# Performance work log

Measured on AMD Instinct MI355X. Metric: run time of the kernel, lower is better.

The kernel has to match this reference:

```python
import jax, jax.numpy as jnp
import numpy as np

N_HIDDEN = 32
RANK = 6
SV_DECAY_GAMMA = 0.3
LEAK_ALPHA = 0.1
INPUT_DIM = 64
OUTPUT_DIM = 32


def setup_inputs() -> dict:
    key = jax.random.key(0)
    ks = jax.random.split(key, 8)
    B, T = 256, 2048
    inputs = jax.random.normal(ks[0], (B, T, INPUT_DIM), dtype=jnp.float32)
    # parameters (match torch init scales)
    m = jax.random.normal(ks[1], (N_HIDDEN, 1), dtype=jnp.float32) * 0.1
    n = jax.random.normal(ks[2], (N_HIDDEN, 1), dtype=jnp.float32) * 0.1
    M = jax.random.normal(ks[3], (N_HIDDEN, RANK), dtype=jnp.float32) * 0.1
    Nmat = jax.random.normal(ks[4], (N_HIDDEN, RANK), dtype=jnp.float32) * 0.1
    # singular-value-decay scaling of M, N (as in _initialize_with_sv_decay)
    target_sv = jnp.exp(-SV_DECAY_GAMMA * jnp.arange(RANK, dtype=jnp.float32))
    target_sv = target_sv / target_sv.sum() * RANK
    sqrt_sv = jnp.sqrt(target_sv)
    M = M * sqrt_sv[None, :]
    Nmat = Nmat * sqrt_sv[None, :]
    bias = jnp.zeros((N_HIDDEN,), dtype=jnp.float32)
    # W_in: Linear(input_dim, N, bias=False) -> weight [N, input_dim]
    lim_in = 1.0 / np.sqrt(INPUT_DIM)
    W_in = jax.random.uniform(ks[5], (N_HIDDEN, INPUT_DIM), minval=-lim_in, maxval=lim_in, dtype=jnp.float32)
    lim_out = 1.0 / np.sqrt(N_HIDDEN)
    W_out = jax.random.uniform(ks[6], (OUTPUT_DIM, N_HIDDEN), minval=-lim_out, maxval=lim_out, dtype=jnp.float32)
    b_out = jax.random.uniform(ks[7], (OUTPUT_DIM,), minval=-lim_out, maxval=lim_out, dtype=jnp.float32)
    return {"inputs": inputs, "W_in": W_in, "m": m, "n": n, "M": M,
            "Nmat": Nmat, "bias": bias, "W_out": W_out, "b_out": b_out}


def reference(inputs, W_in, m, n, M, Nmat, bias, W_out, b_out):
    # h_{t+1} = (1-a) h_t + a * tanh(W_rec h_t + W_in u_t + b); y_t = W_out h_t + b_out
    B, T, _ = inputs.shape
    alpha = LEAK_ALPHA
    # W_rec = m n^T + M N^T (time-invariant; torch recomputes per step, same math)
    W_rec = m @ n.T + M @ Nmat.T                         # [N, N]
    x_proj = jnp.einsum('bti,ni->btn', inputs, W_in)     # [B, T, N]
    h0 = jnp.zeros((B, N_HIDDEN), dtype=inputs.dtype)

    def step(h, x_t):
        pre = h @ W_rec.T + x_t + bias
        h_new = (1.0 - alpha) * h + alpha * jnp.tanh(pre)
        return h_new, h_new

    h_final, hs = jax.lax.scan(step, h0, jnp.swapaxes(x_proj, 0, 1))  # hs: [T, B, N]
    outputs = jnp.einsum('tbn,on->bto', hs, W_out) + b_out            # [B, T, O]
    return outputs, h_final
```

## Files before the change

### kernel.cpp

```cpp
#include <hip/hip_runtime.h>

#define RNN_B 256
#define RNN_T 2048
#define RNN_IN 64
#define RNN_N 32
#define RNN_O 32
#define RNN_R 6
#define RNN_ALPHA 0.1f
#define KSCALE 2.8853900817779268f

__global__ __launch_bounds__(256) void k_xproj(
    const float* __restrict__ u, const float* __restrict__ W_in,
    const float* __restrict__ bias, float* __restrict__ xp)
{
    const int tid = blockIdx.x * 256 + threadIdx.x;
    const float4* __restrict__ u4 =
        reinterpret_cast<const float4*>(u) + (size_t)tid * (RNN_IN / 4);
    float acc[RNN_N];
    #pragma unroll
    for (int n = 0; n < RNN_N; ++n) acc[n] = bias[n];
    #pragma unroll
    for (int q = 0; q < RNN_IN / 4; ++q) {
        const float4 v = u4[q];
        #pragma unroll
        for (int n = 0; n < RNN_N; ++n) {
            const float* wr = W_in + n * RNN_IN + 4 * q;
            acc[n] = fmaf(wr[0], v.x, acc[n]);
            acc[n] = fmaf(wr[1], v.y, acc[n]);
            acc[n] = fmaf(wr[2], v.z, acc[n]);
            acc[n] = fmaf(wr[3], v.w, acc[n]);
        }
    }
    float4* __restrict__ o4 =
        reinterpret_cast<float4*>(xp) + (size_t)tid * (RNN_N / 4);
    #pragma unroll
    for (int q = 0; q < RNN_N / 4; ++q)
        o4[q] = make_float4(KSCALE * acc[4*q+0], KSCALE * acc[4*q+1],
                            KSCALE * acc[4*q+2], KSCALE * acc[4*q+3]);
}

template <int CTRL>
__device__ __forceinline__ float dpp_add(float v) {
    int t = __builtin_amdgcn_update_dpp(0, __float_as_int(v), CTRL, 0xf, 0xf, true);
    return v + __int_as_float(t);
}
__device__ __forceinline__ float sum16(float v) {
    v = dpp_add<0xB1>(v);
    v = dpp_add<0x4E>(v);
    v = dpp_add<0x141>(v);
    v = dpp_add<0x140>(v);
    return v;
}

__device__ __forceinline__ float xsum32(float v) {
#if __has_builtin(__builtin_amdgcn_permlane32_swap)
    typedef int v2i __attribute__((ext_vector_type(2)));
    v2i r = __builtin_amdgcn_permlane32_swap(__float_as_int(v),
                                             __float_as_int(v), false, false);
    return __int_as_float(r.x) + __int_as_float(r.y);
#else
    return v + __shfl_xor(v, 32, 64);
#endif
}
__device__ __forceinline__ float xsum16(float v) {
#if __has_builtin(__builtin_amdgcn_permlane16_swap)
    typedef int v2i __attribute__((ext_vector_type(2)));
    v2i r = __builtin_amdgcn_permlane16_swap(__float_as_int(v),
                                             __float_as_int(v), false, false);
    return __int_as_float(r.x) + __int_as_float(r.y);
#else
    return v + __shfl_xor(v, 16, 64);
#endif
}

__device__ __forceinline__ float fast_exp2(float x) {
#if __has_builtin(__builtin_amdgcn_exp2f)
    return __builtin_amdgcn_exp2f(x);
#else
    return __expf(x * 0.6931471805599453f);
#endif
}
__device__ __forceinline__ float fast_rcp(float x) {
#if __has_builtin(__builtin_amdgcn_rcpf)
    return __builtin_amdgcn_rcpf(x);
#else
    return __frcp_rn(x);
#endif
}

__global__ __launch_bounds__(64, 1) void k_recur(
    const float* __restrict__ m, const float* __restrict__ nvec,
    const float* __restrict__ Mmat, const float* __restrict__ Nmat,
    const float* __restrict__ xp,
    float* __restrict__ hout,
    float* __restrict__ hfin)
{
    const int b    = blockIdx.x;
    const int lane = threadIdx.x;
    const int k    = lane & 15;
    const int q    = (lane >> 4) & 1;
    const int p    = lane >> 5;
    const int e    = 2 * k + p;

    float cn[4], cm[4];
    #pragma unroll
    for (int j = 0; j < 4; ++j) {
        const int r = 4 * q + j;
        float cnv = 0.f, cmv = 0.f;
        if (r == 0)      { cnv = nvec[e];              cmv = m[e]; }
        else if (r <= RNN_R) { cnv = Nmat[e*RNN_R + (r-1)]; cmv = Mmat[e*RNN_R + (r-1)]; }
        cn[j] = cnv;
        cm[j] = KSCALE * cmv;
    }

    const float2* __restrict__ x2 =
        reinterpret_cast<const float2*>(xp + (size_t)b * (RNN_T * RNN_N)) + k;
    float* __restrict__ hbase = hout + (size_t)b * (RNN_T * RNN_N);

    float h = 0.0f;

    const int PF = 8;
    float2 xr[PF];
    #pragma unroll
    for (int i = 0; i < PF; ++i) xr[i] = x2[i * (RNN_N / 2)];

    const bool do_store = (q == 0);

    #pragma unroll 8
    for (int t = 0; t < RNN_T; ++t) {
        const int slot = t & (PF - 1);
        const float2 xv = xr[slot];
        xr[slot] = x2[(t + PF) * (RNN_N / 2)];
        const float xe = p ? xv.y : xv.x;

        float s0 = cn[0] * h, s1 = cn[1] * h, s2 = cn[2] * h, s3 = cn[3] * h;
        s0 = dpp_add<0xB1>(s0);  s1 = dpp_add<0xB1>(s1);
        s2 = dpp_add<0xB1>(s2);  s3 = dpp_add<0xB1>(s3);
        s0 = dpp_add<0x4E>(s0);  s1 = dpp_add<0x4E>(s1);
        s2 = dpp_add<0x4E>(s2);  s3 = dpp_add<0x4E>(s3);
        s0 = dpp_add<0x141>(s0); s1 = dpp_add<0x141>(s1);
        s2 = dpp_add<0x141>(s2); s3 = dpp_add<0x141>(s3);
        s0 = dpp_add<0x140>(s0); s1 = dpp_add<0x140>(s1);
        s2 = dpp_add<0x140>(s2); s3 = dpp_add<0x140>(s3);

        s0 = xsum32(s0); s1 = xsum32(s1); s2 = xsum32(s2); s3 = xsum32(s3);

        float w = fmaf(cm[1], s1, cm[0] * s0) + fmaf(cm[3], s3, cm[2] * s2);
        w = xsum16(w);
        const float z = w + xe;

        const float ez = fast_exp2(z);
        const float g  = fmaf(1.0f - RNN_ALPHA, h, RNN_ALPHA);
        h = fmaf(-2.0f * RNN_ALPHA, fast_rcp(ez + 1.0f), g);

        if (do_store) hbase[t * RNN_N + e] = h;
    }
    if (do_store) hfin[b * RNN_N + e] = h;
}

__global__ __launch_bounds__(256) void k_out(
    const float* __restrict__ W_out, const float* __restrict__ b_out,
    const float* __restrict__ hsrc, float* __restrict__ ydst)
{
    const int tid = blockIdx.x * 256 + threadIdx.x;
    const float4* __restrict__ p4 =
        reinterpret_cast<const float4*>(hsrc) + (size_t)tid * (RNN_N / 4);
    float4* __restrict__ q4 =
        reinterpret_cast<float4*>(ydst) + (size_t)tid * (RNN_N / 4);
    float y[RNN_O];
    #pragma unroll
    for (int o = 0; o < RNN_O; ++o) y[o] = b_out[o];
    #pragma unroll
    for (int q = 0; q < RNN_N / 4; ++q) {
        const float4 v = p4[q];
        #pragma unroll
        for (int o = 0; o < RNN_O; ++o) {
            const float* wr = W_out + o * RNN_N + 4 * q;
            y[o] = fmaf(wr[0], v.x, y[o]);
            y[o] = fmaf(wr[1], v.y, y[o]);
            y[o] = fmaf(wr[2], v.z, y[o]);
            y[o] = fmaf(wr[3], v.w, y[o]);
        }
    }
    #pragma unroll
    for (int q = 0; q < RNN_N / 4; ++q)
        q4[q] = make_float4(y[4*q+0], y[4*q+1], y[4*q+2], y[4*q+3]);
}

extern "C" void kernel_launch(void* const* d_in, const int* in_sizes, int n_in,
                              void* d_out, int out_size, void* d_ws, size_t ws_size,
                              hipStream_t stream)
{
    const float* u     = (const float*)d_in[0];
    const float* W_in  = (const float*)d_in[1];
    const float* m     = (const float*)d_in[2];
    const float* nvec  = (const float*)d_in[3];
    const float* Mmat  = (const float*)d_in[4];
    const float* Nmat  = (const float*)d_in[5];
    const float* bias  = (const float*)d_in[6];
    const float* W_out = (const float*)d_in[7];
    const float* b_out = (const float*)d_in[8];
    float* out = (float*)d_out;

    float* hfin = out + (size_t)RNN_B * RNN_T * RNN_N;

    const size_t hbytes = (size_t)RNN_B * RNN_T * RNN_N * sizeof(float);
    float* hbuf = (ws_size >= hbytes) ? (float*)d_ws : out;

    k_xproj<<<(RNN_B * RNN_T) / 256, 256, 0, stream>>>(u, W_in, bias, out);
    k_recur<<<RNN_B, 64, 0, stream>>>(m, nvec, Mmat, Nmat, out, hbuf, hfin);
    k_out  <<<(RNN_B * RNN_T) / 256, 256, 0, stream>>>(W_out, b_out, hbuf, out);
}
```

Before: 620.9 us.

## Fuse input projection, recurrence and output into one warp-specialized pipelined kernel

Replaces the three-kernel sequence with a single kernel per batch row, where one wavefront computes the input projection for a 64-step chunk into LDS, another runs the recurrence over the previous chunk, and a third computes outputs from the chunk before that. This removes the global round trips for the projected inputs and hidden states and the two extra launches. Only 256 blocks of 4 waves run, with a block-wide barrier per chunk. The recurrence wave may stall waiting for the projection and output waves, and the fourth wave sits idle.

After: 716.9 us. 1.15x slower.

```diff
diff --git a/kernel.cpp b/kernel.cpp
--- a/kernel.cpp
+++ b/kernel.cpp
@@ -8,48 +8,13 @@
 #define RNN_R 6
 #define RNN_ALPHA 0.1f
 #define KSCALE 2.8853900817779268f
-
-__global__ __launch_bounds__(256) void k_xproj(
-    const float* __restrict__ u, const float* __restrict__ W_in,
-    const float* __restrict__ bias, float* __restrict__ xp)
-{
-    const int tid = blockIdx.x * 256 + threadIdx.x;
-    const float4* __restrict__ u4 =
-        reinterpret_cast<const float4*>(u) + (size_t)tid * (RNN_IN / 4);
-    float acc[RNN_N];
-    #pragma unroll
-    for (int n = 0; n < RNN_N; ++n) acc[n] = bias[n];
-    #pragma unroll
-    for (int q = 0; q < RNN_IN / 4; ++q) {
-        const float4 v = u4[q];
-        #pragma unroll
-        for (int n = 0; n < RNN_N; ++n) {
-            const float* wr = W_in + n * RNN_IN + 4 * q;
-            acc[n] = fmaf(wr[0], v.x, acc[n]);
-            acc[n] = fmaf(wr[1], v.y, acc[n]);
-            acc[n] = fmaf(wr[2], v.z, acc[n]);
-            acc[n] = fmaf(wr[3], v.w, acc[n]);
-        }
-    }
-    float4* __restrict__ o4 =
-        reinterpret_cast<float4*>(xp) + (size_t)tid * (RNN_N / 4);
-    #pragma unroll
-    for (int q = 0; q < RNN_N / 4; ++q)
-        o4[q] = make_float4(KSCALE * acc[4*q+0], KSCALE * acc[4*q+1],
-                            KSCALE * acc[4*q+2], KSCALE * acc[4*q+3]);
-}
+#define CHUNK 64
+#define NCH (RNN_T / CHUNK)
 
 template <int CTRL>
 __device__ __forceinline__ float dpp_add(float v) {
     int t = __builtin_amdgcn_update_dpp(0, __float_as_int(v), CTRL, 0xf, 0xf, true);
     return v + __int_as_float(t);
-}
-__device__ __forceinline__ float sum16(float v) {
-    v = dpp_add<0xB1>(v);
-    v = dpp_add<0x4E>(v);
-    v = dpp_add<0x141>(v);
-    v = dpp_add<0x140>(v);
-    return v;
 }
 
 __device__ __forceinline__ float xsum32(float v) {
@@ -88,103 +53,128 @@
 #endif
 }
 
-__global__ __launch_bounds__(64, 1) void k_recur(
+__global__ __launch_bounds__(256, 1) void k_fused(
+    const float* __restrict__ u, const float* __restrict__ W_in,
+    const float* __restrict__ bias,
     const float* __restrict__ m, const float* __restrict__ nvec,
     const float* __restrict__ Mmat, const float* __restrict__ Nmat,
-    const float* __restrict__ xp,
-    float* __restrict__ hout,
-    float* __restrict__ hfin)
+    const float* __restrict__ W_out, const float* __restrict__ b_out,
+    float* __restrict__ yout, float* __restrict__ hfin)
 {
+    __shared__ __align__(16) float xp_lds[2][CHUNK][RNN_N];
+    __shared__ __align__(16) float h_lds[2][CHUNK][RNN_N];
+
     const int b    = blockIdx.x;
-    const int lane = threadIdx.x;
-    const int k    = lane & 15;
-    const int q    = (lane >> 4) & 1;
-    const int p    = lane >> 5;
-    const int e    = 2 * k + p;
+    const int tid  = threadIdx.x;
+    const int wid  = tid >> 6;
+    const int lane = tid & 63;
 
-    float cn[4], cm[4];
-    #pragma unroll
-    for (int j = 0; j < 4; ++j) {
-        const int r = 4 * q + j;
-        float cnv = 0.f, cmv = 0.f;
-        if (r == 0)      { cnv = nvec[e];              cmv = m[e]; }
-        else if (r <= RNN_R) { cnv = Nmat[e*RNN_R + (r-1)]; cmv = Mmat[e*RNN_R + (r-1)]; }
-        cn[j] = cnv;
-        cm[j] = KSCALE * cmv;
+    const int k = lane & 15;
+    const int q = (lane >> 4) & 1;
+    const int p = lane >> 5;
+    const int e = 2 * k + p;
+
+    float cn[4] = {0.f, 0.f, 0.f, 0.f}, cm[4] = {0.f, 0.f, 0.f, 0.f};
+    if (wid == 0) {
+        #pragma unroll
+        for (int j = 0; j < 4; ++j) {
+            const int r = 4 * q + j;
+            float cnv = 0.f, cmv = 0.f;
+            if (r == 0)          { cnv = nvec[e];              cmv = m[e]; }
+            else if (r <= RNN_R) { cnv = Nmat[e*RNN_R + (r-1)]; cmv = Mmat[e*RNN_R + (r-1)]; }
+            cn[j] = cnv;
+            cm[j] = KSCALE * cmv;
+        }
+    }
+    float h = 0.0f;
+    const bool hst = (wid == 0) && (q == 0);
+
+    for (int ph = 0; ph < NCH + 2; ++ph) {
+        if (wid == 1 && ph < NCH) {
+            const int t = ph * CHUNK + lane;
+            const float4* __restrict__ u4 =
+                reinterpret_cast<const float4*>(u) +
+                ((size_t)b * RNN_T + t) * (RNN_IN / 4);
+            float acc[RNN_N];
+            #pragma unroll
+            for (int n = 0; n < RNN_N; ++n) acc[n] = bias[n];
+            #pragma unroll
+            for (int qq = 0; qq < RNN_IN / 4; ++qq) {
+                const float4 v = u4[qq];
+                #pragma unroll
+                for (int n = 0; n < RNN_N; ++n) {
+                    const float* wr = W_in + n * RNN_IN + 4 * qq;
+                    acc[n] = fmaf(wr[0], v.x, acc[n]);
+                    acc[n] = fmaf(wr[1], v.y, acc[n]);
+                    acc[n] = fmaf(wr[2], v.z, acc[n]);
+                    acc[n] = fmaf(wr[3], v.w, acc[n]);
+                }
+            }
+            float4* dst = reinterpret_cast<float4*>(&xp_lds[ph & 1][lane][0]);
+            #pragma unroll
+            for (int qq = 0; qq < RNN_N / 4; ++qq)
+                dst[qq] = make_float4(KSCALE * acc[4*qq+0], KSCALE * acc[4*qq+1],
+                                      KSCALE * acc[4*qq+2], KSCALE * acc[4*qq+3]);
+        } else if (wid == 0 && ph >= 1 && ph <= NCH) {
+            const int buf = (ph - 1) & 1;
+            const float* __restrict__ xrow = &xp_lds[buf][0][e];
+            float*       __restrict__ hrow = &h_lds[buf][0][e];
+            #pragma unroll 8
+            for (int tl = 0; tl < CHUNK; ++tl) {
+                const float xe = xrow[tl * RNN_N];
+
+                float s0 = cn[0]*h, s1 = cn[1]*h, s2 = cn[2]*h, s3 = cn[3]*h;
+                s0 = dpp_add<0xB1>(s0);  s1 = dpp_add<0xB1>(s1);
+                s2 = dpp_add<0xB1>(s2);  s3 = dpp_add<0xB1>(s3);
+                s0 = dpp_add<0x4E>(s0);  s1 = dpp_add<0x4E>(s1);
+                s2 = dpp_add<0x4E>(s2);  s3 = dpp_add<0x4E>(s3);
+                s0 = dpp_add<0x141>(s0); s1 = dpp_add<0x141>(s1);
+                s2 = dpp_add<0x141>(s2); s3 = dpp_add<0x141>(s3);
+                s0 = dpp_add<0x140>(s0); s1 = dpp_add<0x140>(s1);
+                s2 = dpp_add<0x140>(s2); s3 = dpp_add<0x140>(s3);
+
+                s0 = xsum32(s0); s1 = xsum32(s1); s2 = xsum32(s2); s3 = xsum32(s3);
+
+                float w = fmaf(cm[1], s1, cm[0]*s0) + fmaf(cm[3], s3, cm[2]*s2);
+                w = xsum16(w);
+                const float z = w + xe;
+
+                const float ez = fast_exp2(z);
+                const float g  = fmaf(1.0f - RNN_ALPHA, h, RNN_ALPHA);
+                h = fmaf(-2.0f * RNN_ALPHA, fast_rcp(ez + 1.0f), g);
+
+                if (hst) hrow[tl * RNN_N] = h;
+            }
+        } else if (wid == 2 && ph >= 2) {
+            const int ch = ph - 2;
+            const int t  = ch * CHUNK + lane;
+            const float4* __restrict__ hr =
+                reinterpret_cast<const float4*>(&h_lds[ch & 1][lane][0]);
+            float y[RNN_O];
+            #pragma unroll
+            for (int o = 0; o < RNN_O; ++o) y[o] = b_out[o];
+            #pragma unroll
+            for (int qq = 0; qq < RNN_N / 4; ++qq) {
+                const float4 v = hr[qq];
+                #pragma unroll
+                for (int o = 0; o < RNN_O; ++o) {
+                    const float* wr = W_out + o * RNN_N + 4 * qq;
+                    y[o] = fmaf(wr[0], v.x, y[o]);
+                    y[o] = fmaf(wr[1], v.y, y[o]);
+                    y[o] = fmaf(wr[2], v.z, y[o]);
+                    y[o] = fmaf(wr[3], v.w, y[o]);
+                }
+            }
+            float4* q4 = reinterpret_cast<float4*>(yout) +
+                         ((size_t)b * RNN_T + t) * (RNN_N / 4);
+            #pragma unroll
+            for (int qq = 0; qq < RNN_N / 4; ++qq)
+                q4[qq] = make_float4(y[4*qq+0], y[4*qq+1], y[4*qq+2], y[4*qq+3]);
+        }
+        __syncthreads();
     }
 
-    const float2* __restrict__ x2 =
-        reinterpret_cast<const float2*>(xp + (size_t)b * (RNN_T * RNN_N)) + k;
-    float* __restrict__ hbase = hout + (size_t)b * (RNN_T * RNN_N);
-
-    float h = 0.0f;
-
-    const int PF = 8;
-    float2 xr[PF];
-    #pragma unroll
-    for (int i = 0; i < PF; ++i) xr[i] = x2[i * (RNN_N / 2)];
-
-    const bool do_store = (q == 0);
-
-    #pragma unroll 8
-    for (int t = 0; t < RNN_T; ++t) {
-        const int slot = t & (PF - 1);
-        const float2 xv = xr[slot];
-        xr[slot] = x2[(t + PF) * (RNN_N / 2)];
-        const float xe = p ? xv.y : xv.x;
-
-        float s0 = cn[0] * h, s1 = cn[1] * h, s2 = cn[2] * h, s3 = cn[3] * h;
-        s0 = dpp_add<0xB1>(s0);  s1 = dpp_add<0xB1>(s1);
-        s2 = dpp_add<0xB1>(s2);  s3 = dpp_add<0xB1>(s3);
-        s0 = dpp_add<0x4E>(s0);  s1 = dpp_add<0x4E>(s1);
-        s2 = dpp_add<0x4E>(s2);  s3 = dpp_add<0x4E>(s3);
-        s0 = dpp_add<0x141>(s0); s1 = dpp_add<0x141>(s1);
-        s2 = dpp_add<0x141>(s2); s3 = dpp_add<0x141>(s3);
-        s0 = dpp_add<0x140>(s0); s1 = dpp_add<0x140>(s1);
-        s2 = dpp_add<0x140>(s2); s3 = dpp_add<0x140>(s3);
-
-        s0 = xsum32(s0); s1 = xsum32(s1); s2 = xsum32(s2); s3 = xsum32(s3);
-
-        float w = fmaf(cm[1], s1, cm[0] * s0) + fmaf(cm[3], s3, cm[2] * s2);
-        w = xsum16(w);
-        const float z = w + xe;
-
-        const float ez = fast_exp2(z);
-        const float g  = fmaf(1.0f - RNN_ALPHA, h, RNN_ALPHA);
-        h = fmaf(-2.0f * RNN_ALPHA, fast_rcp(ez + 1.0f), g);
-
-        if (do_store) hbase[t * RNN_N + e] = h;
-    }
-    if (do_store) hfin[b * RNN_N + e] = h;
-}
-
-__global__ __launch_bounds__(256) void k_out(
-    const float* __restrict__ W_out, const float* __restrict__ b_out,
-    const float* __restrict__ hsrc, float* __restrict__ ydst)
-{
-    const int tid = blockIdx.x * 256 + threadIdx.x;
-    const float4* __restrict__ p4 =
-        reinterpret_cast<const float4*>(hsrc) + (size_t)tid * (RNN_N / 4);
-    float4* __restrict__ q4 =
-        reinterpret_cast<float4*>(ydst) + (size_t)tid * (RNN_N / 4);
-    float y[RNN_O];
-    #pragma unroll
-    for (int o = 0; o < RNN_O; ++o) y[o] = b_out[o];
-    #pragma unroll
-    for (int q = 0; q < RNN_N / 4; ++q) {
-        const float4 v = p4[q];
-        #pragma unroll
-        for (int o = 0; o < RNN_O; ++o) {
-            const float* wr = W_out + o * RNN_N + 4 * q;
-            y[o] = fmaf(wr[0], v.x, y[o]);
-            y[o] = fmaf(wr[1], v.y, y[o]);
-            y[o] = fmaf(wr[2], v.z, y[o]);
-            y[o] = fmaf(wr[3], v.w, y[o]);
-        }
-    }
-    #pragma unroll
-    for (int q = 0; q < RNN_N / 4; ++q)
-        q4[q] = make_float4(y[4*q+0], y[4*q+1], y[4*q+2], y[4*q+3]);
+    if (hst) hfin[b * RNN_N + e] = h;
 }
 
 extern "C" void kernel_launch(void* const* d_in, const int* in_sizes, int n_in,
@@ -204,10 +194,6 @@
 
     float* hfin = out + (size_t)RNN_B * RNN_T * RNN_N;
 
-    const size_t hbytes = (size_t)RNN_B * RNN_T * RNN_N * sizeof(float);
-    float* hbuf = (ws_size >= hbytes) ? (float*)d_ws : out;
-
-    k_xproj<<<(RNN_B * RNN_T) / 256, 256, 0, stream>>>(u, W_in, bias, out);
-    k_recur<<<RNN_B, 64, 0, stream>>>(m, nvec, Mmat, Nmat, out, hbuf, hfin);
-    k_out  <<<(RNN_B * RNN_T) / 256, 256, 0, stream>>>(W_out, b_out, hbuf, out);
+    k_fused<<<RNN_B, 256, 0, stream>>>(u, W_in, bias, m, nvec, Mmat, Nmat,
+                                       W_out, b_out, out, hfin);
 }
```
